# Kernel optimization log

Measured on AMD Instinct MI355X. Metric: run time of the kernel, lower is better.

## Reference

```python
import jax, jax.numpy as jnp
from jax import lax
import numpy as np

B, N, C = 16, 2048, 512


def setup_inputs() -> dict:
    key = jax.random.key(0)
    ks = jax.random.split(key, 9)
    s1 = (2.0 / C) ** 0.5   # kaiming fan_in for k=1 convs
    s3 = (2.0 / (3 * C)) ** 0.5  # kaiming fan_in for k=3 convs
    return {
        "x": jax.random.normal(ks[0], (B, N, C), jnp.float32),
        "w1_q": jax.random.normal(ks[1], (C, C), jnp.float32) * s1,
        "w3_q": jax.random.normal(ks[2], (C, C, 3), jnp.float32) * s3,
        "w1_k": jax.random.normal(ks[3], (C, C), jnp.float32) * s1,
        "w3_k": jax.random.normal(ks[4], (C, C, 3), jnp.float32) * s3,
        "w1_v": jax.random.normal(ks[5], (C, C), jnp.float32) * s1,
        "w3_v": jax.random.normal(ks[6], (C, C, 3), jnp.float32) * s3,
        "w_proj": jax.random.normal(ks[7], (C, C), jnp.float32) * s1,
        "b_proj": jax.random.normal(ks[8], (C,), jnp.float32) * 0.01,
    }


def _qkv_branch(xc, w1, w3):
    # xc: [B, C, N]; conv1d k=1 (no bias) then conv1d k=3, circular pad 1 (no bias)
    h = jnp.einsum("oc,bcn->bon", w1, xc)
    hp = jnp.pad(h, ((0, 0), (0, 0), (1, 1)), mode="wrap")
    return lax.conv_general_dilated(
        hp, w3, window_strides=(1,), padding="VALID",
        dimension_numbers=("NCH", "OIH", "NCH"))  # [B, C, N]


def reference(x, w1_q, w3_q, w1_k, w3_k, w1_v, w3_v, w_proj, b_proj):
    # x: [B, N, C]
    xc = jnp.transpose(x, (0, 2, 1))  # [B, C, N]
    q = _qkv_branch(xc, w1_q, w3_q)
    k = _qkv_branch(xc, w1_k, w3_k)
    v = _qkv_branch(xc, w1_v, w3_v)
    # channel attention: scores are [B, C, C]; scale applied twice = 1/d_model
    scale2 = 1.0 / C
    attn = jnp.einsum("bcn,bdn->bcd", q, k) * scale2
    attn = jax.nn.softmax(attn, axis=-1)
    out = jnp.einsum("bcd,bdn->bcn", attn, v)  # [B, C, N]
    y = jnp.einsum("oc,bcn->bon", w_proj, out) + b_proj[None, :, None]
    return jnp.transpose(y, (0, 2, 1))  # [B, N, C]
```

## Files before the change

### kernel.cpp

```cpp
#include <hip/hip_runtime.h>
#include <hip/hip_bf16.h>
#include <hip/hip_fp16.h>
#include <stdint.h>

typedef __bf16 bf16;
typedef __bf16 bf16x8 __attribute__((ext_vector_type(8)));
typedef _Float16 f16x8 __attribute__((ext_vector_type(8)));
typedef float f32x4 __attribute__((ext_vector_type(4)));

#define NSEQ 2048
#define CDIM 512

#define WS_FLAGS   0
#define WS_BPB     1024
#define WS_WPB     4096
#define WS_WEC     532480
#define WS_WECT    3678208
#define WS_W1T     5251072
#define WS_W3R     6823936
#define WS_BASE    11542528

__device__ __forceinline__ float rdf(const void* p, long i, int f) {
  if (f == 1) return ((const float*)p)[i];
  if (f == 2) return (float)((const _Float16*)p)[i];
  return (float)((const bf16*)p)[i];
}

__device__ __forceinline__ void gl_lds16(const bf16* g, bf16* l) {
  __builtin_amdgcn_global_load_lds(
      (__attribute__((address_space(1))) void*)g,
      (__attribute__((address_space(3))) void*)l, 16, 0, 0);
}

__device__ __forceinline__ void stage_one(const void* gb, long eoff, int dt,
                                          bf16* ldst)
{
  if (dt == 1) {
    const float* g = (const float*)gb + eoff;
    const float4 u0 = *(const float4*)g;
    const float4 u1 = *(const float4*)(g + 4);
    bf16x8 t;
    t[0]=(bf16)u0.x; t[1]=(bf16)u0.y; t[2]=(bf16)u0.z; t[3]=(bf16)u0.w;
    t[4]=(bf16)u1.x; t[5]=(bf16)u1.y; t[6]=(bf16)u1.z; t[7]=(bf16)u1.w;
    *(bf16x8*)ldst = t;
  } else if (dt == 2) {
    const f16x8 h = *(const f16x8*)((const _Float16*)gb + eoff);
    bf16x8 t;
#pragma unroll
    for (int j = 0; j < 8; ++j) t[j] = (bf16)(float)h[j];
    *(bf16x8*)ldst = t;
  } else {
    gl_lds16((const bf16*)gb + eoff, ldst);
  }
}

__global__ __launch_bounds__(256)
void detect2(const unsigned short* __restrict__ a,
             const unsigned short* __restrict__ b, int* __restrict__ flags)
{
  const unsigned short* p = blockIdx.x ? b : a;
  __shared__ int chi, clo;
  if (threadIdx.x == 0) { chi = 0; clo = 0; }
  __syncthreads();
  int hi = 0, lo = 0;
  for (int i = threadIdx.x; i < 4096; i += 256) {
    const int e = (p[i] >> 7) & 0xff;
    hi += (e >= 141);
    lo += (e >= 1 && e <= 110);
  }
  atomicAdd(&chi, hi);
  atomicAdd(&clo, lo);
  __syncthreads();
  if (threadIdx.x == 0) {
    flags[blockIdx.x] = (chi > 8) ? 1 : ((clo > 100) ? 2 : 0);
    if (blockIdx.x == 0) flags[2] = 0;
  }
}

__global__ __launch_bounds__(256)
void cvt_x8(const void* __restrict__ x, const int* __restrict__ flag,
            bf16* __restrict__ xb)
{
  const long i8 = (long)blockIdx.x * 256 + threadIdx.x;
  const int f = *flag;
  bf16x8 t;
  if (f == 1) {
    const float4* g = (const float4*)x + i8 * 2;
    const float4 u0 = g[0], u1 = g[1];
    t[0]=(bf16)u0.x; t[1]=(bf16)u0.y; t[2]=(bf16)u0.z; t[3]=(bf16)u0.w;
    t[4]=(bf16)u1.x; t[5]=(bf16)u1.y; t[6]=(bf16)u1.z; t[7]=(bf16)u1.w;
  } else if (f == 2) {
    const f16x8 h = ((const f16x8*)x)[i8];
#pragma unroll
    for (int j = 0; j < 8; ++j) t[j] = (bf16)(float)h[j];
  } else {
    t = ((const bf16x8*)x)[i8];
  }
  ((bf16x8*)xb)[i8] = t;
}

template<int AX3, int BX3, int EPI, int ZMODE>
__global__ __launch_bounds__(256)
void gemm_bt(const void* __restrict__ Abase, const void* __restrict__ Bbase,
             void* __restrict__ Cbase, const bf16* __restrict__ bias,
             const int* __restrict__ xflag, int zxb,
             int M, int Nd, int K, int lda, int ldb, int ldc,
             long zsA, long zsB, long zsC)
{
  __shared__ bf16 As[128 * 32];
  __shared__ bf16 Bs[128 * 32];
  const int z = blockIdx.z;
  const int xdt = (AX3 || BX3) ? *xflag : 0;
  long Aoff, Boff; char* CB;
  if (ZMODE == 1) {
    const int g = z / 3, t = z - g * 3;
    Aoff = (long)z * 262144;
    Boff = (long)g * 262144;
    CB = (char*)Cbase + ((long)g * (512 * 1536) + t * 512) * 2;
  } else {
    Aoff = AX3 ? 0 : (long)z * zsA;
    Boff = BX3 ? 0 : (long)z * zsB;
    CB = (char*)Cbase + (long)z * zsC * (EPI == 2 ? 4 : 2);
  }
  const int m0 = blockIdx.y * 128;
  const int n0 = blockIdx.x * 128;
  const int tid = threadIdx.x;
  const int lane = tid & 63;
  const int w = tid >> 6;
  const int wr = (w >> 1) * 64;
  const int wc = (w & 1) * 64;

  f32x4 acc[4][4];
  const f32x4 zero = {0.f, 0.f, 0.f, 0.f};
#pragma unroll
  for (int i = 0; i < 4; ++i)
#pragma unroll
    for (int j = 0; j < 4; ++j) acc[i][j] = zero;

  for (int k0 = 0; k0 < K; k0 += 32) {
#pragma unroll
    for (int it = 0; it < 2; ++it) {
      const int f  = (it * 256 + tid) * 16;
      const int r  = f >> 6;
      const int cb = (f & 63) >> 1;
      long ea, eb;
      if (AX3) {
        const int tau = k0 >> 9;
        ea = (long)(z + zxb) * zsA +
             (long)((m0 + r + tau - 1) & (NSEQ - 1)) * CDIM + (k0 & 511) + cb;
      } else {
        ea = Aoff + (long)(m0 + r) * lda + k0 + cb;
      }
      stage_one(Abase, ea, AX3 ? xdt : 0, (bf16*)((char*)As + f));
      if (BX3) {
        const int tau = k0 >> 9;
        eb = (long)(z + zxb) * zsB +
             (long)((n0 + r + tau - 1) & (NSEQ - 1)) * CDIM + (k0 & 511) + cb;
      } else {
        eb = Boff + (long)(n0 + r) * ldb + k0 + cb;
      }
      stage_one(Bbase, eb, BX3 ? xdt : 0, (bf16*)((char*)Bs + f));
    }
    __syncthreads();

    const int qb = (lane >> 4) * 16;
    const int fr = lane & 15;
    bf16x8 af[4], bfr[4];
#pragma unroll
    for (int i = 0; i < 4; ++i)
      af[i] = *(const bf16x8*)((const char*)As + (wr + i * 16 + fr) * 64 + qb);
#pragma unroll
    for (int j = 0; j < 4; ++j)
      bfr[j] = *(const bf16x8*)((const char*)Bs + (wc + j * 16 + fr) * 64 + qb);
#pragma unroll
    for (int i = 0; i < 4; ++i)
#pragma unroll
      for (int j = 0; j < 4; ++j)
        acc[i][j] = __builtin_amdgcn_mfma_f32_16x16x32_bf16(af[i], bfr[j], acc[i][j], 0, 0, 0);
    __syncthreads();
  }

  const int qa4 = (lane >> 4) * 4;
  const int cn = lane & 15;
#pragma unroll
  for (int i = 0; i < 4; ++i) {
#pragma unroll
    for (int j = 0; j < 4; ++j) {
      const int gn = n0 + wc + j * 16 + cn;
      const float bv = (EPI == 2) ? (float)bias[gn] : 0.f;
#pragma unroll
      for (int r = 0; r < 4; ++r) {
        const long gm = m0 + wr + i * 16 + qa4 + r;
        if (EPI == 2) ((float*)CB)[gm * ldc + gn] = acc[i][j][r] + bv;
        else          ((bf16*)CB)[gm * ldc + gn] = (bf16)acc[i][j][r];
      }
    }
  }
}

template<int X3>
__device__ __forceinline__ void stage32(const bf16* __restrict__ gb, long zoff,
                                        int r0, int k0, int ld,
                                        char* ldsb, int tid)
{
#pragma unroll
  for (int is = 0; is < 2; ++is) {
    const int c = is * 512 + tid;
    const int g = c >> 6;
    const int l = c & 63;
    const int r = g * 16 + (l & 15);
    const int kb = l >> 4;
    long e;
    if (X3) {
      const int tau = k0 >> 9;
      const int rg = (r0 + r + tau - 1) & (NSEQ - 1);
      e = zoff + (long)rg * CDIM + ((k0 & 511) + kb * 8);
    } else {
      e = zoff + (long)(r0 + r) * ld + k0 + kb * 8;
    }
    gl_lds16(gb + e, (bf16*)(ldsb + c * 16));
  }
}

template<int AX3, int BX3, int EPI>
__global__ __launch_bounds__(512)
void gemm8(const bf16* __restrict__ Ab, const bf16* __restrict__ Bb,
           void* __restrict__ Cbase, const bf16* __restrict__ bias,
           int zxb, int M, int Nd, int K, int lda, int ldb, int ldc,
           long zsA, long zsB, long zsC)
{
  __shared__ char smem[65536];
  const int z = blockIdx.z;
  const long Aoff = (long)(AX3 ? (z + zxb) : z) * zsA;
  const long Boff = (long)(BX3 ? (z + zxb) : z) * zsB;
  char* CB = (char*)Cbase + (long)z * zsC * (EPI == 2 ? 4 : 2);
  const int m0 = blockIdx.y * 256;
  const int n0 = blockIdx.x * 256;
  const int tid = threadIdx.x;
  const int lane = tid & 63;
  const int w = tid >> 6, wm = w >> 2, wn = w & 3;
  const int fro = lane * 16;

  f32x4 acc[8][4];
  const f32x4 zero = {0.f, 0.f, 0.f, 0.f};
#pragma unroll
  for (int i = 0; i < 8; ++i)
#pragma unroll
    for (int j = 0; j < 4; ++j) acc[i][j] = zero;

  const int KT = K >> 5;

  stage32<AX3>(Ab, Aoff, m0, 0, lda, smem, tid);
  stage32<BX3>(Bb, Boff, n0, 0, ldb, smem + 16384, tid);
  __syncthreads();

  for (int T = 0; T < KT; ++T) {
    const int cur = T & 1;
    const char* sA = smem + cur * 32768;
    const char* sB = sA + 16384;

    if (T + 1 < KT) {
      char* nb = smem + (cur ^ 1) * 32768;
      const int k1 = (T + 1) << 5;
      stage32<AX3>(Ab, Aoff, m0, k1, lda, nb, tid);
      stage32<BX3>(Bb, Boff, n0, k1, ldb, nb + 16384, tid);
    }

    bf16x8 bfr[4];
#pragma unroll
    for (int j = 0; j < 4; ++j)
      bfr[j] = *(const bf16x8*)(sB + (wn * 4 + j) * 1024 + fro);

#pragma unroll
    for (int h = 0; h < 2; ++h) {
      bf16x8 af[4];
#pragma unroll
      for (int i2 = 0; i2 < 4; ++i2)
        af[i2] = *(const bf16x8*)(sA + (wm * 8 + h * 4 + i2) * 1024 + fro);
      __builtin_amdgcn_s_setprio(1);
#pragma unroll
      for (int i2 = 0; i2 < 4; ++i2)
#pragma unroll
        for (int j = 0; j < 4; ++j)
          acc[h * 4 + i2][j] = __builtin_amdgcn_mfma_f32_16x16x32_bf16(
              af[i2], bfr[j], acc[h * 4 + i2][j], 0, 0, 0);
      __builtin_amdgcn_s_setprio(0);
      if (h == 0) __builtin_amdgcn_s_barrier();
    }
    __syncthreads();
  }

  const int lr = lane & 15, lk = lane >> 4;
#pragma unroll
  for (int i = 0; i < 8; ++i) {
#pragma unroll
    for (int j = 0; j < 4; ++j) {
      const int gn = n0 + wn * 64 + j * 16 + lr;
      const float bv = (EPI == 2) ? (float)bias[gn] : 0.f;
#pragma unroll
      for (int r = 0; r < 4; ++r) {
        const long gm = m0 + wm * 128 + i * 16 + lk * 4 + r;
        if (EPI == 2) ((float*)CB)[gm * ldc + gn] = acc[i][j][r] + bv;
        else          ((bf16*)CB)[gm * ldc + gn] = (bf16)acc[i][j][r];
      }
    }
  }
}

__global__ __launch_bounds__(256)
void repack(const void* __restrict__ w1q, const void* __restrict__ w3q,
            const void* __restrict__ w1k, const void* __restrict__ w3k,
            const void* __restrict__ w1v, const void* __restrict__ w3v,
            const void* __restrict__ wp, const void* __restrict__ bpr,
            const int* __restrict__ flag,
            bf16* __restrict__ w1t, bf16* __restrict__ w3r,
            bf16* __restrict__ wpb, bf16* __restrict__ bpb)
{
  const int isf = *flag;
  const int g = blockIdx.z;
  const void* w1 = (g == 0) ? w1q : (g == 1) ? w1k : w1v;
  const void* w3 = (g == 0) ? w3q : (g == 1) ? w3k : w3v;
  const int idx = blockIdx.x * 256 + threadIdx.x;
  const int o = idx >> 9, c = idx & 511;
  w1t[g * 262144 + idx] = (bf16)rdf(w1, (long)c * 512 + o, isf);
#pragma unroll
  for (int t = 0; t < 3; ++t)
    w3r[(g * 3 + t) * 262144 + idx] = (bf16)rdf(w3, ((long)o * 512 + c) * 3 + t, isf);
  if (g == 0) {
    wpb[idx] = (bf16)rdf(wp, idx, isf);
    if (idx < 512) bpb[idx] = (bf16)rdf(bpr, idx, isf);
  }
}

__global__ __launch_bounds__(256)
void softmax_cols(bf16* __restrict__ S)
{
  const int b = blockIdx.z;
  const int c = blockIdx.x * 256 + threadIdx.x;
  bf16* s = S + (long)b * 262144 + c;
  const float sc = 1.0f / 512.0f;
  float m = -3.4e38f, l = 0.f;
  for (int d = 0; d < 512; ++d) {
    const float v = (float)s[d * 512] * sc;
    const float nm = fmaxf(m, v);
    l = l * __expf(m - nm) + __expf(v - nm);
    m = nm;
  }
  const float inv = 1.0f / l;
  for (int d = 0; d < 512; ++d) {
    const float v = (float)s[d * 512] * sc;
    s[d * 512] = (bf16)(__expf(v - m) * inv);
  }
}

extern "C" void kernel_launch(void* const* d_in, const int* in_sizes, int n_in,
                              void* d_out, int out_size, void* d_ws, size_t ws_size,
                              hipStream_t stream)
{
  long smax = -1, smin = (long)1 << 62;
  for (int i = 0; i < n_in; ++i) {
    const long s = in_sizes[i];
    if (s > smax) smax = s;
    if (s < smin) smin = s;
  }
  long s3 = -1;
  for (int i = 0; i < n_in; ++i) {
    const long s = in_sizes[i];
    if (s < smax && s > s3) s3 = s;
  }
  int xi = -1, bi = -1, w1i[8], n1 = 0, w3i[8], n3 = 0;
  for (int i = 0; i < n_in; ++i) {
    const long s = in_sizes[i];
    if (s == smax && xi < 0) xi = i;
    else if (s == smin && bi < 0) bi = i;
    else if (s == s3) { if (n3 < 8) w3i[n3++] = i; }
    else             { if (n1 < 8) w1i[n1++] = i; }
  }
  const void *x, *w1q, *w3q, *w1k, *w3k, *w1v, *w3v, *wp, *bp;
  if (xi >= 0 && bi >= 0 && n1 >= 4 && n3 >= 3) {
    x = d_in[xi]; bp = d_in[bi];
    w1q = d_in[w1i[0]]; w1k = d_in[w1i[1]]; w1v = d_in[w1i[2]]; wp = d_in[w1i[3]];
    w3q = d_in[w3i[0]]; w3k = d_in[w3i[1]]; w3v = d_in[w3i[2]];
  } else {
    x = d_in[0]; w1q = d_in[1]; w3q = d_in[2]; w1k = d_in[3]; w3k = d_in[4];
    w1v = d_in[5]; w3v = d_in[6]; wp = d_in[7]; bp = d_in[8];
  }
  float* out = (float*)d_out;

  char* ws = (char*)d_ws;
  int*  flags = (int*)(ws + WS_FLAGS);
  bf16* bpb  = (bf16*)(ws + WS_BPB);
  bf16* wpb  = (bf16*)(ws + WS_WPB);
  bf16* wec  = (bf16*)(ws + WS_WEC);
  bf16* wecT = (bf16*)(ws + WS_WECT);
  bf16* w1t  = (bf16*)(ws + WS_W1T);
  bf16* w3r  = (bf16*)(ws + WS_W3R);

  int NB = 16, conv = 1;
  while (NB >= 1 && WS_BASE + (size_t)NB * 2621440 + 33554432 > ws_size) NB >>= 1;
  if (NB == 0) {
    conv = 0; NB = 16;
    while (NB > 1 && WS_BASE + (size_t)NB * 2621440 > ws_size) NB >>= 1;
  }
  bf16* Sb    = (bf16*)(ws + WS_BASE);
  bf16* slotA = (bf16*)(ws + WS_BASE + (size_t)NB * 524288);
  bf16* U     = slotA;
  bf16* Wfin  = slotA + (size_t)NB * 262144;
  bf16* xb    = (bf16*)(ws + WS_BASE + (size_t)NB * 2621440);

  const dim3 blk(256, 1, 1);
  const dim3 blk8(512, 1, 1);

  detect2<<<dim3(2, 1, 1), blk, 0, stream>>>(
      (const unsigned short*)x, (const unsigned short*)w1q, flags);

  const void* xu = x;
  const int* xflag = flags;
  if (conv) {
    cvt_x8<<<dim3(8192, 1, 1), blk, 0, stream>>>(x, flags, xb);
    xu = xb;
    xflag = flags + 2;
  }

  repack<<<dim3(1024, 1, 3), blk, 0, stream>>>(w1q, w3q, w1k, w3k, w1v, w3v,
                                               wp, bp, flags + 1,
                                               w1t, w3r, wpb, bpb);
  gemm_bt<0, 0, 0, 1><<<dim3(4, 4, 6), blk, 0, stream>>>(
      w3r, w1t, wec, nullptr, nullptr, 0, 512, 512, 512, 512, 512, 1536, 0, 0, 0);
  gemm_bt<0, 0, 0, 0><<<dim3(4, 4, 3), blk, 0, stream>>>(
      w1t + 2 * 262144, w3r + 6 * 262144, wecT, nullptr, nullptr, 0,
      512, 512, 512, 512, 512, 512, 0, 262144, 262144);

  for (int b0 = 0; b0 < 16; b0 += NB) {
    char* outc = (char*)out + (size_t)b0 * 2048 * 512 * 4;
    if (conv) {
      bf16* QKc = (bf16*)outc;
      gemm8<0, 1, 0><<<dim3(8, 4, NB), blk8, 0, stream>>>(
          wec, (const bf16*)xu, QKc, nullptr, b0,
          1024, 2048, 1536, 1536, 0, 2048,
          0, (long)NSEQ * CDIM, (long)1024 * 2048);
      gemm_bt<0, 0, 0, 0><<<dim3(4, 4, NB), blk, 0, stream>>>(
          QKc + (long)512 * 2048, QKc, Sb, nullptr, nullptr, 0,
          512, 512, 2048, 2048, 2048, 512,
          (long)1024 * 2048, (long)1024 * 2048, (long)512 * 512);
      softmax_cols<<<dim3(2, 1, NB), blk, 0, stream>>>(Sb);
      gemm_bt<0, 0, 0, 0><<<dim3(4, 4, NB), blk, 0, stream>>>(
          wpb, Sb, U, nullptr, nullptr, 0, 512, 512, 512, 512, 512, 512,
          0, (long)512 * 512, (long)512 * 512);
      gemm8<0, 0, 0><<<dim3(6, 2, NB), blk8, 0, stream>>>(
          U, wecT, Wfin, nullptr, 0, 512, 1536, 512, 512, 512, 1536,
          (long)512 * 512, 0, (long)512 * 1536);
      gemm8<1, 0, 2><<<dim3(2, 8, NB), blk8, 0, stream>>>(
          (const bf16*)xu, Wfin, outc, bpb, b0,
          2048, 512, 1536, 0, 1536, 512,
          (long)NSEQ * CDIM, (long)512 * 1536, (long)2048 * 512);
    } else {
      bf16* Kc = (bf16*)outc;
      gemm_bt<0, 1, 0, 0><<<dim3(16, 4, NB), blk, 0, stream>>>(
          wec, xu, slotA, nullptr, xflag, b0, 512, 2048, 1536, 1536, 0, 2048,
          0, (long)NSEQ * CDIM, (long)512 * 2048);
      gemm_bt<0, 1, 0, 0><<<dim3(16, 4, NB), blk, 0, stream>>>(
          wec + 512 * 1536, xu, Kc, nullptr, xflag, b0, 512, 2048, 1536, 1536, 0, 2048,
          0, (long)NSEQ * CDIM, (long)512 * 2048);
      gemm_bt<0, 0, 0, 0><<<dim3(4, 4, NB), blk, 0, stream>>>(
          Kc, slotA, Sb, nullptr, nullptr, 0, 512, 512, 2048, 2048, 2048, 512,
          (long)512 * 2048, (long)512 * 2048, (long)512 * 512);
      softmax_cols<<<dim3(2, 1, NB), blk, 0, stream>>>(Sb);
      gemm_bt<0, 0, 0, 0><<<dim3(4, 4, NB), blk, 0, stream>>>(
          wpb, Sb, U, nullptr, nullptr, 0, 512, 512, 512, 512, 512, 512,
          0, (long)512 * 512, (long)512 * 512);
      gemm_bt<0, 0, 0, 0><<<dim3(12, 4, NB), blk, 0, stream>>>(
          U, wecT, Wfin, nullptr, nullptr, 0, 512, 1536, 512, 512, 512, 1536,
          (long)512 * 512, 0, (long)512 * 1536);
      gemm_bt<1, 0, 2, 0><<<dim3(4, 16, NB), blk, 0, stream>>>(
          xu, Wfin, outc, bpb, xflag, b0,
          2048, 512, 1536, 0, 1536, 512,
          (long)NSEQ * CDIM, (long)512 * 1536, (long)2048 * 512);
    }
  }
}
```

Baseline: 518.6 us.

## Add triple-buffered XCD-swizzled GEMM and split column softmax into two passes

Adds a gemm8p kernel that keeps three LDS stages in flight, using vmcnt-based waits instead of a full syncthreads per K step. It also remaps block indices so consecutive tiles land on the same XCD for better L2 reuse. The column softmax is split into a partial max/sum pass and a normalize pass across four row chunks, which raises parallelism from a few dozen blocks. In exchange it needs 96KB dynamic shared memory, which lowers occupancy, and it adds an extra kernel launch and partials traffic.

```diff
diff --git a/kernel.cpp b/kernel.cpp
--- a/kernel.cpp
+++ b/kernel.cpp
@@ -249,7 +249,6 @@
     for (int j = 0; j < 4; ++j) acc[i][j] = zero;
 
   const int KT = K >> 5;
-
   stage32<AX3>(Ab, Aoff, m0, 0, lda, smem, tid);
   stage32<BX3>(Bb, Boff, n0, 0, ldb, smem + 16384, tid);
   __syncthreads();
@@ -258,19 +257,16 @@
     const int cur = T & 1;
     const char* sA = smem + cur * 32768;
     const char* sB = sA + 16384;
-
     if (T + 1 < KT) {
       char* nb = smem + (cur ^ 1) * 32768;
       const int k1 = (T + 1) << 5;
       stage32<AX3>(Ab, Aoff, m0, k1, lda, nb, tid);
       stage32<BX3>(Bb, Boff, n0, k1, ldb, nb + 16384, tid);
     }
-
     bf16x8 bfr[4];
 #pragma unroll
     for (int j = 0; j < 4; ++j)
       bfr[j] = *(const bf16x8*)(sB + (wn * 4 + j) * 1024 + fro);
-
 #pragma unroll
     for (int h = 0; h < 2; ++h) {
       bf16x8 af[4];
@@ -302,6 +298,101 @@
         const long gm = m0 + wm * 128 + i * 16 + lk * 4 + r;
         if (EPI == 2) ((float*)CB)[gm * ldc + gn] = acc[i][j][r] + bv;
         else          ((bf16*)CB)[gm * ldc + gn] = (bf16)acc[i][j][r];
+      }
+    }
+  }
+}
+
+template<int AX3, int BX3, int EPI>
+__global__ __launch_bounds__(512)
+void gemm8p(const bf16* __restrict__ Ab, const bf16* __restrict__ Bb,
+            void* __restrict__ Cbase, const bf16* __restrict__ bias,
+            int zxb, int M, int Nd, int K, int lda, int ldb, int ldc,
+            long zsA, long zsB, long zsC)
+{
+  extern __shared__ char smem[];
+  const int gx = gridDim.x, gy = gridDim.y;
+  const int total = gx * gy * gridDim.z;
+  const int lin = blockIdx.x + gx * (blockIdx.y + gy * blockIdx.z);
+  const int q = total >> 3, r = total & 7;
+  const int xcd = lin & 7, k = lin >> 3;
+  int swz = (xcd < r ? xcd * (q + 1) : r * (q + 1) + (xcd - r) * q) + k;
+  const int ny = swz % gy; swz /= gy;
+  const int nx = swz % gx;
+  const int z  = swz / gx;
+
+  const long Aoff = (long)(AX3 ? (z + zxb) : z) * zsA;
+  const long Boff = (long)(BX3 ? (z + zxb) : z) * zsB;
+  char* CB = (char*)Cbase + (long)z * zsC * (EPI == 2 ? 4 : 2);
+  const int m0 = ny * 256;
+  const int n0 = nx * 256;
+  const int tid = threadIdx.x;
+  const int lane = tid & 63;
+  const int w = tid >> 6, wm = w >> 2, wn = w & 3;
+  const int fro = lane * 16;
+
+  f32x4 acc[8][4];
+  const f32x4 zero = {0.f, 0.f, 0.f, 0.f};
+#pragma unroll
+  for (int i = 0; i < 8; ++i)
+#pragma unroll
+    for (int j = 0; j < 4; ++j) acc[i][j] = zero;
+
+  const int KT = K >> 5;
+
+  stage32<AX3>(Ab, Aoff, m0, 0, lda, smem, tid);
+  stage32<BX3>(Bb, Boff, n0, 0, ldb, smem + 16384, tid);
+  stage32<AX3>(Ab, Aoff, m0, 32, lda, smem + 32768, tid);
+  stage32<BX3>(Bb, Boff, n0, 32, ldb, smem + 32768 + 16384, tid);
+
+  for (int T = 0; T < KT; ++T) {
+    if (T + 1 < KT) asm volatile("s_waitcnt vmcnt(4)" ::: "memory");
+    else            asm volatile("s_waitcnt vmcnt(0)" ::: "memory");
+    __builtin_amdgcn_s_barrier();
+
+    if (T + 2 < KT) {
+      char* nb = smem + ((T + 2) % 3) * 32768;
+      const int k2 = (T + 2) << 5;
+      stage32<AX3>(Ab, Aoff, m0, k2, lda, nb, tid);
+      stage32<BX3>(Bb, Boff, n0, k2, ldb, nb + 16384, tid);
+    }
+
+    const char* sA = smem + (T % 3) * 32768;
+    const char* sB = sA + 16384;
+    bf16x8 bfr[4];
+#pragma unroll
+    for (int j = 0; j < 4; ++j)
+      bfr[j] = *(const bf16x8*)(sB + (wn * 4 + j) * 1024 + fro);
+#pragma unroll
+    for (int h = 0; h < 2; ++h) {
+      bf16x8 af[4];
+#pragma unroll
+      for (int i2 = 0; i2 < 4; ++i2)
+        af[i2] = *(const bf16x8*)(sA + (wm * 8 + h * 4 + i2) * 1024 + fro);
+      __builtin_amdgcn_s_setprio(1);
+#pragma unroll
+      for (int i2 = 0; i2 < 4; ++i2)
+#pragma unroll
+        for (int j = 0; j < 4; ++j)
+          acc[h * 4 + i2][j] = __builtin_amdgcn_mfma_f32_16x16x32_bf16(
+              af[i2], bfr[j], acc[h * 4 + i2][j], 0, 0, 0);
+      __builtin_amdgcn_s_setprio(0);
+      if (h == 0) __builtin_amdgcn_s_barrier();
+    }
+  }
+
+  const int lr = lane & 15, lk = lane >> 4;
+#pragma unroll
+  for (int i = 0; i < 8; ++i) {
+#pragma unroll
+    for (int j = 0; j < 4; ++j) {
+      const int gn = n0 + wn * 64 + j * 16 + lr;
+      const float bv = (EPI == 2) ? (float)bias[gn] : 0.f;
+#pragma unroll
+      for (int r2 = 0; r2 < 4; ++r2) {
+        const long gm = m0 + wm * 128 + i * 16 + lk * 4 + r2;
+        if (EPI == 2) ((float*)CB)[gm * ldc + gn] = acc[i][j][r2] + bv;
+        else          ((bf16*)CB)[gm * ldc + gn] = (bf16)acc[i][j][r2];
       }
     }
   }
@@ -333,21 +424,41 @@
 }
 
 __global__ __launch_bounds__(256)
-void softmax_cols(bf16* __restrict__ S)
-{
-  const int b = blockIdx.z;
+void softmax_p1(const bf16* __restrict__ S, float2* __restrict__ P)
+{
+  const int z = blockIdx.z;
   const int c = blockIdx.x * 256 + threadIdx.x;
-  bf16* s = S + (long)b * 262144 + c;
+  const int d0 = blockIdx.y * 128;
+  const bf16* s = S + (long)z * 262144 + c;
   const float sc = 1.0f / 512.0f;
   float m = -3.4e38f, l = 0.f;
-  for (int d = 0; d < 512; ++d) {
+  for (int d = d0; d < d0 + 128; ++d) {
     const float v = (float)s[d * 512] * sc;
     const float nm = fmaxf(m, v);
     l = l * __expf(m - nm) + __expf(v - nm);
     m = nm;
   }
+  P[((long)z * 4 + blockIdx.y) * 512 + c] = make_float2(m, l);
+}
+
+__global__ __launch_bounds__(256)
+void softmax_p2(bf16* __restrict__ S, const float2* __restrict__ P)
+{
+  const int z = blockIdx.z;
+  const int c = blockIdx.x * 256 + threadIdx.x;
+  const int d0 = blockIdx.y * 128;
+  float m = -3.4e38f, l = 0.f;
+#pragma unroll
+  for (int i = 0; i < 4; ++i) {
+    const float2 p = P[((long)z * 4 + i) * 512 + c];
+    const float nm = fmaxf(m, p.x);
+    l = l * __expf(m - nm) + p.y * __expf(p.x - nm);
+    m = nm;
+  }
   const float inv = 1.0f / l;
-  for (int d = 0; d < 512; ++d) {
+  bf16* s = S + (long)z * 262144 + c;
+  const float sc = 1.0f / 512.0f;
+  for (int d = d0; d < d0 + 128; ++d) {
     const float v = (float)s[d * 512] * sc;
     s[d * 512] = (bf16)(__expf(v - m) * inv);
   }
@@ -407,9 +518,24 @@
   bf16* U     = slotA;
   bf16* Wfin  = slotA + (size_t)NB * 262144;
   bf16* xb    = (bf16*)(ws + WS_BASE + (size_t)NB * 2621440);
+  float2* Pp  = (float2*)slotA;
 
   const dim3 blk(256, 1, 1);
   const dim3 blk8(512, 1, 1);
+
+  bool ok8 = true;
+  {
+    hipError_t e;
+    e = hipFuncSetAttribute(reinterpret_cast<const void*>(&gemm8p<0, 1, 0>),
+                            hipFuncAttributeMaxDynamicSharedMemorySize, 98304);
+    ok8 = ok8 && (e == hipSuccess);
+    e = hipFuncSetAttribute(reinterpret_cast<const void*>(&gemm8p<0, 0, 0>),
+                            hipFuncAttributeMaxDynamicSharedMemorySize, 98304);
+    ok8 = ok8 && (e == hipSuccess);
+    e = hipFuncSetAttribute(reinterpret_cast<const void*>(&gemm8p<1, 0, 2>),
+                            hipFuncAttributeMaxDynamicSharedMemorySize, 98304);
+    ok8 = ok8 && (e == hipSuccess);
+  }
 
   detect2<<<dim3(2, 1, 1), blk, 0, stream>>>(
       (const unsigned short*)x, (const unsigned short*)w1q, flags);
@@ -435,25 +561,43 @@
     char* outc = (char*)out + (size_t)b0 * 2048 * 512 * 4;
     if (conv) {
       bf16* QKc = (bf16*)outc;
-      gemm8<0, 1, 0><<<dim3(8, 4, NB), blk8, 0, stream>>>(
-          wec, (const bf16*)xu, QKc, nullptr, b0,
-          1024, 2048, 1536, 1536, 0, 2048,
-          0, (long)NSEQ * CDIM, (long)1024 * 2048);
+      if (ok8) {
+        gemm8p<0, 1, 0><<<dim3(8, 4, NB), blk8, 98304, stream>>>(
+            wec, (const bf16*)xu, QKc, nullptr, b0,
+            1024, 2048, 1536, 1536, 0, 2048,
+            0, (long)NSEQ * CDIM, (long)1024 * 2048);
+      } else {
+        gemm8<0, 1, 0><<<dim3(8, 4, NB), blk8, 0, stream>>>(
+            wec, (const bf16*)xu, QKc, nullptr, b0,
+            1024, 2048, 1536, 1536, 0, 2048,
+            0, (long)NSEQ * CDIM, (long)1024 * 2048);
+      }
       gemm_bt<0, 0, 0, 0><<<dim3(4, 4, NB), blk, 0, stream>>>(
           QKc + (long)512 * 2048, QKc, Sb, nullptr, nullptr, 0,
           512, 512, 2048, 2048, 2048, 512,
           (long)1024 * 2048, (long)1024 * 2048, (long)512 * 512);
-      softmax_cols<<<dim3(2, 1, NB), blk, 0, stream>>>(Sb);
+      softmax_p1<<<dim3(2, 4, NB), blk, 0, stream>>>(Sb, Pp);
+      softmax_p2<<<dim3(2, 4, NB), blk, 0, stream>>>(Sb, Pp);
       gemm_bt<0, 0, 0, 0><<<dim3(4, 4, NB), blk, 0, stream>>>(
           wpb, Sb, U, nullptr, nullptr, 0, 512, 512, 512, 512, 512, 512,
           0, (long)512 * 512, (long)512 * 512);
-      gemm8<0, 0, 0><<<dim3(6, 2, NB), blk8, 0, stream>>>(
-          U, wecT, Wfin, nullptr, 0, 512, 1536, 512, 512, 512, 1536,
-          (long)512 * 512, 0, (long)512 * 1536);
-      gemm8<1, 0, 2><<<dim3(2, 8, NB), blk8, 0, stream>>>(
-          (const bf16*)xu, Wfin, outc, bpb, b0,
-          2048, 512, 1536, 0, 1536, 512,
-          (long)NSEQ * CDIM, (long)512 * 1536, (long)2048 * 512);
+      if (ok8) {
+        gemm8p<0, 0, 0><<<dim3(6, 2, NB), blk8, 98304, stream>>>(
+            U, wecT, Wfin, nullptr, 0, 512, 1536, 512, 512, 512, 1536,
+            (long)512 * 512, 0, (long)512 * 1536);
+        gemm8p<1, 0, 2><<<dim3(2, 8, NB), blk8, 98304, stream>>>(
+            (const bf16*)xu, Wfin, outc, bpb, b0,
+            2048, 512, 1536, 0, 1536, 512,
+            (long)NSEQ * CDIM, (long)512 * 1536, (long)2048 * 512);
+      } else {
+        gemm8<0, 0, 0><<<dim3(6, 2, NB), blk8, 0, stream>>>(
+            U, wecT, Wfin, nullptr, 0, 512, 1536, 512, 512, 512, 1536,
+            (long)512 * 512, 0, (long)512 * 1536);
+        gemm8<1, 0, 2><<<dim3(2, 8, NB), blk8, 0, stream>>>(
+            (const bf16*)xu, Wfin, outc, bpb, b0,
+            2048, 512, 1536, 0, 1536, 512,
+            (long)NSEQ * CDIM, (long)512 * 1536, (long)2048 * 512);
+      }
     } else {
       bf16* Kc = (bf16*)outc;
       gemm_bt<0, 1, 0, 0><<<dim3(16, 4, NB), blk, 0, stream>>>(
@@ -465,7 +609,8 @@
       gemm_bt<0, 0, 0, 0><<<dim3(4, 4, NB), blk, 0, stream>>>(
           Kc, slotA, Sb, nullptr, nullptr, 0, 512, 512, 2048, 2048, 2048, 512,
           (long)512 * 2048, (long)512 * 2048, (long)512 * 512);
-      softmax_cols<<<dim3(2, 1, NB), blk, 0, stream>>>(Sb);
+      softmax_p1<<<dim3(2, 4, NB), blk, 0, stream>>>(Sb, Pp);
+      softmax_p2<<<dim3(2, 4, NB), blk, 0, stream>>>(Sb, Pp);
       gemm_bt<0, 0, 0, 0><<<dim3(4, 4, NB), blk, 0, stream>>>(
           wpb, Sb, U, nullptr, nullptr, 0, 512, 512, 512, 512, 512, 512,
           0, (long)512 * 512, (long)512 * 512);
```

Measured after the change: 437.9 us. 1.18x faster.
